# Performance work log

Measured on AMD Instinct MI355X. Metric: run time of the kernel, lower is better.

The kernel has to match this reference:

```python
import math
import jax, jax.numpy as jnp
import numpy as np

D_MODEL = 1024
N_HEADS = 16
D_K = D_MODEL // N_HEADS
THETA = 10000.0
B, S = 2, 2048


def setup_inputs() -> dict:
    key = jax.random.key(0)
    k1, k2, k3 = jax.random.split(key, 3)
    x = jax.random.normal(k1, (B, S, D_MODEL), dtype=jnp.float32)
    token_positions = jnp.arange(B * S, dtype=jnp.int32).reshape(B, S)
    std_qkv = math.sqrt(2.0 / (D_MODEL + 3 * D_MODEL))
    std_o = math.sqrt(2.0 / (D_MODEL + D_MODEL))
    W_qkv = jax.random.truncated_normal(k2, -3.0, 3.0, (3 * D_MODEL, D_MODEL), dtype=jnp.float32) * std_qkv
    W_o = jax.random.truncated_normal(k3, -3.0, 3.0, (D_MODEL, D_MODEL), dtype=jnp.float32) * std_o
    return {"x": x, "W_qkv": W_qkv, "W_o": W_o, "token_positions": token_positions}


def _rope(x, pos):
    # x: (B, H, S, D_K); pos: (B, S) int
    half = D_K // 2
    inv_freq = 1.0 / (THETA ** (jnp.arange(0, D_K, 2, dtype=jnp.float32) / D_K))  # (half,)
    # pos_extended = pos[:, None, :] -> freqs (B, 1, S, half)
    freqs = pos[:, None, :, None].astype(jnp.float32) * inv_freq
    cos, sin = jnp.cos(freqs), jnp.sin(freqs)
    xr = x.reshape(*x.shape[:-1], half, 2)
    x1, x2 = xr[..., 0], xr[..., 1]
    out = jnp.stack([x1 * cos - x2 * sin, x2 * cos + x1 * sin], axis=-1)
    return out.reshape(x.shape)


def reference(x, W_qkv, W_o, token_positions):
    seq_len = x.shape[-2]
    qkv = jnp.einsum('bsi,oi->bso', x, W_qkv)
    q, k, v = jnp.split(qkv, 3, axis=-1)
    # (B, S, H*D) -> (B, H, S, D)
    def to_heads(t):
        return t.reshape(t.shape[0], t.shape[1], N_HEADS, D_K).transpose(0, 2, 1, 3)
    q, k, v = to_heads(q), to_heads(k), to_heads(v)
    q = _rope(q, token_positions)
    k = _rope(k, token_positions)
    scores = jnp.einsum('bhnd,bhmd->bhnm', q, k) / math.sqrt(D_K)
    causal = jnp.tril(jnp.ones((seq_len, seq_len), dtype=bool))
    scores = jnp.where(causal, scores, -jnp.inf)
    attn = jax.nn.softmax(scores, axis=-1)
    out = jnp.einsum('bhnm,bhmd->bhnd', attn, v)
    out = out.transpose(0, 2, 1, 3).reshape(x.shape[0], seq_len, D_MODEL)
    return jnp.einsum('bsi,oi->bso', out, W_o)
```

## Files before the change

kernel.cpp:

```cpp
#include <hip/hip_runtime.h>
#include <cmath>

typedef __bf16 bf16;
typedef bf16 bf16x4 __attribute__((ext_vector_type(4)));
typedef bf16 bf16x8 __attribute__((ext_vector_type(8)));
typedef float f32x4 __attribute__((ext_vector_type(4)));

#define MFMA16(a, b, c) __builtin_amdgcn_mfma_f32_16x16x32_bf16(a, b, c, 0, 0, 0)

#define GLOAD16(g, l)                                                   \
  __builtin_amdgcn_global_load_lds(                                     \
      (const __attribute__((address_space(1))) unsigned int*)(g),       \
      (__attribute__((address_space(3))) unsigned int*)(l), 16, 0, 0)

__global__ __launch_bounds__(256) void cvt_all(
    const float* __restrict__ x, const float* __restrict__ wqkv,
    const float* __restrict__ wo, bf16* __restrict__ xb,
    bf16* __restrict__ wqkvb, bf16* __restrict__ wob) {
  int i = (blockIdx.x * 256 + threadIdx.x) * 4;
  const float* src;
  bf16* dst;
  if (i < (4 << 20)) {
    src = x + i; dst = xb + i;
  } else if (i < (7 << 20)) {
    src = wqkv + (i - (4 << 20)); dst = wqkvb + (i - (4 << 20));
  } else {
    src = wo + (i - (7 << 20)); dst = wob + (i - (7 << 20));
  }
  const f32x4 v = *(const f32x4*)src;
  bf16x4 o = {(bf16)v[0], (bf16)v[1], (bf16)v[2], (bf16)v[3]};
  *(bf16x4*)dst = o;
}

template <int EPI, int BN>
__global__ __launch_bounds__(256) void gemm_nt(
    const bf16* __restrict__ A, const bf16* __restrict__ Bm,
    const int* __restrict__ tokpos,
    bf16* __restrict__ out0, bf16* __restrict__ out1, bf16* __restrict__ out2,
    float* __restrict__ outF, int N) {
  constexpr int NI = BN / 32;
  constexpr int TSTRIDE = 136;
  __shared__ __align__(16) union SMem {
    struct { bf16 A[2][128 * 32]; bf16 B[2][BN * 32]; } st;
    bf16 T[EPI ? 128 * TSTRIDE : 1];
  } sm;
  const int tid = threadIdx.x;
  const int w = tid >> 6, lane = tid & 63, quad = lane >> 4, m16 = lane & 15;
  const int nwg = gridDim.x * gridDim.y;
  int bid = blockIdx.y * gridDim.x + blockIdx.x;
  bid = (bid & 7) * (nwg >> 3) + (bid >> 3);
  const int m0 = (bid / gridDim.x) * 128, n0 = (bid % gridDim.x) * BN;
  const int wm = (w >> 1) * 64, wn = (w & 1) * (BN / 2);

  f32x4 acc[4][NI] = {};

  const int row0 = tid >> 2, ch = tid & 3;
  const bf16* Ag0 = A + (size_t)(m0 + row0) * 1024 + ch * 8;
  const bf16* Ag1 = Ag0 + (size_t)64 * 1024;
  const bf16* Bg0 = Bm + (size_t)(n0 + row0) * 1024 + ch * 8;
  const bf16* Bg1 = Bg0 + (size_t)64 * 1024;

  auto STAGE = [&](int p, int k0) {
    GLOAD16(Ag0 + k0, &sm.st.A[p][tid * 8]);
    GLOAD16(Ag1 + k0, &sm.st.A[p][2048 + tid * 8]);
    GLOAD16(Bg0 + k0, &sm.st.B[p][tid * 8]);
    if constexpr (BN == 128) GLOAD16(Bg1 + k0, &sm.st.B[p][2048 + tid * 8]);
  };

  STAGE(0, 0);
  __syncthreads();

  int p = 0;
  for (int k0 = 0; k0 < 1024; k0 += 32) {
    const bool more = (k0 + 32) < 1024;
    if (more) STAGE(p ^ 1, k0 + 32);
    bf16x8 af[4], bfr[NI];
#pragma unroll
    for (int mi = 0; mi < 4; ++mi)
      af[mi] =
          *(const bf16x8*)(&sm.st.A[p][(wm + mi * 16 + m16) * 32 + quad * 8]);
#pragma unroll
    for (int ni = 0; ni < NI; ++ni)
      bfr[ni] =
          *(const bf16x8*)(&sm.st.B[p][(wn + ni * 16 + m16) * 32 + quad * 8]);
#pragma unroll
    for (int mi = 0; mi < 4; ++mi)
#pragma unroll
      for (int ni = 0; ni < NI; ++ni)
        acc[mi][ni] = MFMA16(af[mi], bfr[ni], acc[mi][ni]);
    if (more) {
      __syncthreads();
      p ^= 1;
    }
  }

  if constexpr (EPI == 0) {
#pragma unroll
    for (int mi = 0; mi < 4; ++mi) {
      int rowb = m0 + wm + mi * 16 + quad * 4;
#pragma unroll
      for (int r = 0; r < 4; ++r) {
        size_t off = (size_t)(rowb + r) * N + n0 + wn;
#pragma unroll
        for (int ni = 0; ni < NI; ++ni)
          outF[off + ni * 16 + m16] = acc[mi][ni][r];
      }
    }
  } else {
    const int secb = n0 >> 10;
    if (secb == 2) {
      __syncthreads();
#pragma unroll
      for (int mi = 0; mi < 4; ++mi) {
        int rlb = wm + mi * 16 + quad * 4;
#pragma unroll
        for (int ni = 0; ni < 4; ++ni) {
          int c = wn + ni * 16 + m16;
          bf16x4 pk = {(bf16)acc[mi][ni][0], (bf16)acc[mi][ni][1],
                       (bf16)acc[mi][ni][2], (bf16)acc[mi][ni][3]};
          *(bf16x4*)(&sm.T[c * TSTRIDE + rlb]) = pk;
        }
      }
      __syncthreads();
      const int bb = m0 >> 11, S0 = m0 & 2047;
      const size_t base = ((size_t)bb * 1024 + (n0 - 2048)) * 2048 + S0;
#pragma unroll
      for (int it = 0; it < 8; ++it) {
        int chunk = it * 256 + tid;
        int c = chunk >> 4, kp = (chunk & 15) * 8;
        bf16x8 v = *(const bf16x8*)(&sm.T[c * TSTRIDE + kp]);
        *(bf16x8*)(out2 + base + (size_t)c * 2048 + kp) = v;
      }
    } else {
      bf16* dst = secb ? out1 : out0;
      const float sc = secb ? 1.0f : 0.125f;
#pragma unroll
      for (int mi = 0; mi < 4; ++mi) {
        int rowb = m0 + wm + mi * 16 + quad * 4;
        int pos4[4];
#pragma unroll
        for (int r = 0; r < 4; ++r) pos4[r] = tokpos[rowb + r];
#pragma unroll
        for (int ni = 0; ni < 4; ++ni) {
          int col = n0 + wn + ni * 16 + m16;
          int f = col & 1023, h = f >> 6, d = f & 63;
          float inv = __expf(-(float)(d & ~1) * (9.2103403719762f / 64.f));
#pragma unroll
          for (int r = 0; r < 4; ++r) {
            float v = acc[mi][ni][r];
            float vp = __shfl_xor(v, 1);
            float ang = (float)pos4[r] * inv;
            float cs, sn;
            __sincosf(ang, &sn, &cs);
            float ov = (d & 1) ? (v * cs + vp * sn) : (v * cs - vp * sn);
            ov *= sc;
            int row = rowb + r;
            int bb = row >> 11, s = row & 2047;
            dst[((size_t)(bb * 16 + h) * 2048 + s) * 64 + d] = (bf16)ov;
          }
        }
      }
    }
  }
}

__global__ __launch_bounds__(256) void attn_kernel(
    const bf16* __restrict__ Q, const bf16* __restrict__ K,
    const bf16* __restrict__ Vt, bf16* __restrict__ O) {
  __shared__ __align__(16) bf16 KP[2][64 * 64];
  __shared__ __align__(16) bf16 VP[2][64 * 64];
  __shared__ __align__(16) bf16 PS[4][16 * 64];
  const int tid = threadIdx.x;
  const int w = tid >> 6, lane = tid & 63, quad = lane >> 4, m16 = lane & 15;
  const int h8 = m16 >> 3, ml = m16 & 7;
  const int bh = blockIdx.x;
  const int j = 31 - blockIdx.y;
  const bf16* Qb = Q + (size_t)bh * 2048 * 64;
  const bf16* Kb = K + (size_t)bh * 2048 * 64;
  const bf16* Vb = Vt + (size_t)bh * 64 * 2048;

  const int srow = tid >> 3, sc = (tid & 7) ^ (srow & 7);
  const bf16* Kg = Kb + (size_t)srow * 64 + sc * 8;
  const bf16* Vg = Vb + (size_t)srow * 2048 + sc * 8;
  auto GSTAGE = [&](int kt, int p) {
    const bf16* kg = Kg + (size_t)kt * 4096;
    const bf16* vg = Vg + kt * 64;
    GLOAD16(kg, &KP[p][tid * 8]);
    GLOAD16(kg + (size_t)32 * 64, &KP[p][2048 + tid * 8]);
    GLOAD16(vg, &VP[p][tid * 8]);
    GLOAD16(vg + (size_t)32 * 2048, &VP[p][2048 + tid * 8]);
  };

  const bf16* qrow = Qb + (size_t)(j * 64 + w * 16 + m16) * 64;
  bf16x8 aq[2];
  aq[0] = *(const bf16x8*)(qrow + quad * 8);
  aq[1] = *(const bf16x8*)(qrow + 32 + quad * 8);

  GSTAGE(0, 0);
  __syncthreads();

  f32x4 o[4] = {};
  float l4[4] = {0.f, 0.f, 0.f, 0.f};
  const int qrel = w * 16 + quad * 4;
  bf16* ps = PS[w];

  int p = 0;
  for (int kt = 0; kt <= j; ++kt) {
    const bool more = kt < j;
    if (more) GSTAGE(kt + 1, p ^ 1);

    f32x4 sa[4] = {};
    __builtin_amdgcn_s_setprio(1);
#pragma unroll
    for (int kk = 0; kk < 2; ++kk)
#pragma unroll
      for (int ni = 0; ni < 4; ++ni) {
        bf16x8 bk = *(const bf16x8*)(
            &KP[p][(ni * 16 + m16) * 64 + (((kk * 4 + quad) ^ ml) << 3)]);
        sa[ni] = MFMA16(aq[kk], bk, sa[ni]);
      }
    __builtin_amdgcn_s_setprio(0);

    const bool diag = (kt == j);
#pragma unroll
    for (int r = 0; r < 4; ++r) {
      const int prow = quad * 4 + r;
      const int rb = prow * 64, rx = prow & 7;
#pragma unroll
      for (int ni = 0; ni < 4; ++ni) {
        float pp = exp2f(fmaf(sa[ni][r], 1.44269504f, -11.5415603f));
        if (diag && (ni * 16 + m16) > qrel + r) pp = 0.f;
        l4[r] += pp;
        ps[rb + (((ni * 2 + h8) ^ rx) << 3) + ml] = (bf16)pp;
      }
    }
    bf16x8 ap[2];
#pragma unroll
    for (int kk = 0; kk < 2; ++kk)
      ap[kk] =
          *(const bf16x8*)(&ps[m16 * 64 + (((kk * 4 + quad) ^ ml) << 3)]);
    __builtin_amdgcn_s_setprio(1);
#pragma unroll
    for (int kk = 0; kk < 2; ++kk)
#pragma unroll
      for (int ng = 0; ng < 4; ++ng) {
        bf16x8 bv = *(const bf16x8*)(
            &VP[p][(ng * 16 + m16) * 64 + (((kk * 4 + quad) ^ ml) << 3)]);
        o[ng] = MFMA16(ap[kk], bv, o[ng]);
      }
    __builtin_amdgcn_s_setprio(0);

    if (more) {
      __syncthreads();
      p ^= 1;
    }
  }

  const int b = bh >> 4, hh = bh & 15;
#pragma unroll
  for (int r = 0; r < 4; ++r) {
    float l = l4[r];
    l += __shfl_xor(l, 1);
    l += __shfl_xor(l, 2);
    l += __shfl_xor(l, 4);
    l += __shfl_xor(l, 8);
    float inv_l = 1.f / l;
    int s = j * 64 + w * 16 + quad * 4 + r;
    size_t rowoff = (size_t)(b * 2048 + s) * 1024 + hh * 64;
#pragma unroll
    for (int ng = 0; ng < 4; ++ng)
      O[rowoff + ng * 16 + m16] = (bf16)(o[ng][r] * inv_l);
  }
}

extern "C" void kernel_launch(void* const* d_in, const int* in_sizes, int n_in,
                              void* d_out, int out_size, void* d_ws, size_t ws_size,
                              hipStream_t stream) {
  (void)in_sizes; (void)n_in; (void)out_size; (void)ws_size;
  const float* x = (const float*)d_in[0];
  const float* Wqkv = (const float*)d_in[1];
  const float* Wo = (const float*)d_in[2];
  const int* tokpos = (const int*)d_in[3];
  float* out = (float*)d_out;

  const size_t NEL = (size_t)2 * 16 * 2048 * 64;
  bf16* Qws = (bf16*)d_ws;
  bf16* Kws = Qws + NEL;
  bf16* Vtw = Kws + NEL;
  bf16* Ows = Vtw + NEL;
  bf16* xb  = Ows + NEL;
  bf16* Wqkvb = xb + NEL;
  bf16* Wob = Wqkvb + (size_t)3072 * 1024;

  cvt_all<<<8192, 256, 0, stream>>>(x, Wqkv, Wo, xb, Wqkvb, Wob);

  gemm_nt<1, 128><<<dim3(24, 32), 256, 0, stream>>>(xb, Wqkvb, tokpos, Qws,
                                                    Kws, Vtw, nullptr, 3072);
  attn_kernel<<<dim3(32, 32), 256, 0, stream>>>(Qws, Kws, Vtw, Ows);
  gemm_nt<0, 64><<<dim3(16, 32), 256, 0, stream>>>(Ows, Wob, nullptr, nullptr,
                                                   nullptr, nullptr, out, 1024);
}
```

Baseline: 176.9 us.

## Precompute RoPE cos/sin table and stage Q/K epilogue through LDS for vector stores

The conversion kernel gains extra blocks that precompute a cos/sin table indexed by position and frequency, written into the attention-output workspace before that buffer is used. The QKV GEMM epilogue reads this table instead of calling exp and sincos per element. It then writes rotated Q/K values into shared memory and emits coalesced 16-byte stores per head row, replacing scattered 2-byte stores. The trade-off is extra table reads and two barriers. The table assumes positions below 4096, since it is sized for 4096 positions × 32 frequencies.

```diff
diff --git a/kernel.cpp b/kernel.cpp
--- a/kernel.cpp
+++ b/kernel.cpp
@@ -16,7 +16,17 @@
 __global__ __launch_bounds__(256) void cvt_all(
     const float* __restrict__ x, const float* __restrict__ wqkv,
     const float* __restrict__ wo, bf16* __restrict__ xb,
-    bf16* __restrict__ wqkvb, bf16* __restrict__ wob) {
+    bf16* __restrict__ wqkvb, bf16* __restrict__ wob,
+    float2* __restrict__ tab) {
+  if (blockIdx.x >= 8192) {
+    int id = (blockIdx.x - 8192) * 256 + threadIdx.x;
+    int pos = id >> 5, dh = id & 31;
+    float ang = (float)pos * __expf(-(float)dh * 0.28782313662425572f);
+    float sn, cs;
+    __sincosf(ang, &sn, &cs);
+    tab[id] = make_float2(cs, sn);
+    return;
+  }
   int i = (blockIdx.x * 256 + threadIdx.x) * 4;
   const float* src;
   bf16* dst;
@@ -35,7 +45,7 @@
 template <int EPI, int BN>
 __global__ __launch_bounds__(256) void gemm_nt(
     const bf16* __restrict__ A, const bf16* __restrict__ Bm,
-    const int* __restrict__ tokpos,
+    const int* __restrict__ tokpos, const float2* __restrict__ tab,
     bf16* __restrict__ out0, bf16* __restrict__ out1, bf16* __restrict__ out2,
     float* __restrict__ outF, int N) {
   constexpr int NI = BN / 32;
@@ -108,6 +118,7 @@
     }
   } else {
     const int secb = n0 >> 10;
+    const int bb = m0 >> 11, S0 = m0 & 2047;
     if (secb == 2) {
       __syncthreads();
 #pragma unroll
@@ -122,7 +133,6 @@
         }
       }
       __syncthreads();
-      const int bb = m0 >> 11, S0 = m0 & 2047;
       const size_t base = ((size_t)bb * 1024 + (n0 - 2048)) * 2048 + S0;
 #pragma unroll
       for (int it = 0; it < 8; ++it) {
@@ -132,33 +142,40 @@
         *(bf16x8*)(out2 + base + (size_t)c * 2048 + kp) = v;
       }
     } else {
+      __syncthreads();
       bf16* dst = secb ? out1 : out0;
       const float sc = secb ? 1.0f : 0.125f;
 #pragma unroll
       for (int mi = 0; mi < 4; ++mi) {
-        int rowb = m0 + wm + mi * 16 + quad * 4;
+        int rlb = wm + mi * 16 + quad * 4;
         int pos4[4];
 #pragma unroll
-        for (int r = 0; r < 4; ++r) pos4[r] = tokpos[rowb + r];
+        for (int r = 0; r < 4; ++r) pos4[r] = tokpos[m0 + rlb + r];
 #pragma unroll
         for (int ni = 0; ni < 4; ++ni) {
-          int col = n0 + wn + ni * 16 + m16;
-          int f = col & 1023, h = f >> 6, d = f & 63;
-          float inv = __expf(-(float)(d & ~1) * (9.2103403719762f / 64.f));
+          int c = wn + ni * 16 + m16;
+          int dh = (c & 63) >> 1;
 #pragma unroll
           for (int r = 0; r < 4; ++r) {
             float v = acc[mi][ni][r];
             float vp = __shfl_xor(v, 1);
-            float ang = (float)pos4[r] * inv;
-            float cs, sn;
-            __sincosf(ang, &sn, &cs);
-            float ov = (d & 1) ? (v * cs + vp * sn) : (v * cs - vp * sn);
-            ov *= sc;
-            int row = rowb + r;
-            int bb = row >> 11, s = row & 2047;
-            dst[((size_t)(bb * 16 + h) * 2048 + s) * 64 + d] = (bf16)ov;
+            float2 cssn = tab[pos4[r] * 32 + dh];
+            float ov = (c & 1) ? (v * cssn.x + vp * cssn.y)
+                               : (v * cssn.x - vp * cssn.y);
+            sm.T[(rlb + r) * TSTRIDE + c] = (bf16)(ov * sc);
           }
         }
+      }
+      __syncthreads();
+      const int hbase = (n0 & 1023) >> 6;
+#pragma unroll
+      for (int it = 0; it < 8; ++it) {
+        int chunk = it * 256 + tid;
+        int sl = chunk >> 4, part = chunk & 15;
+        int h = hbase + (part >> 3), d0 = (part & 7) * 8;
+        bf16x8 v = *(const bf16x8*)(&sm.T[sl * TSTRIDE + part * 8]);
+        *(bf16x8*)(dst + ((size_t)(bb * 16 + h) * 2048 + S0 + sl) * 64 + d0) =
+            v;
       }
     }
   }
@@ -291,12 +308,15 @@
   bf16* xb  = Ows + NEL;
   bf16* Wqkvb = xb + NEL;
   bf16* Wob = Wqkvb + (size_t)3072 * 1024;
-
-  cvt_all<<<8192, 256, 0, stream>>>(x, Wqkv, Wo, xb, Wqkvb, Wob);
-
-  gemm_nt<1, 128><<<dim3(24, 32), 256, 0, stream>>>(xb, Wqkvb, tokpos, Qws,
-                                                    Kws, Vtw, nullptr, 3072);
+  float2* tab = (float2*)Ows;
+
+  cvt_all<<<8704, 256, 0, stream>>>(x, Wqkv, Wo, xb, Wqkvb, Wob, tab);
+
+  gemm_nt<1, 128><<<dim3(24, 32), 256, 0, stream>>>(xb, Wqkvb, tokpos, tab,
+                                                    Qws, Kws, Vtw, nullptr,
+                                                    3072);
   attn_kernel<<<dim3(32, 32), 256, 0, stream>>>(Qws, Kws, Vtw, Ows);
   gemm_nt<0, 64><<<dim3(16, 32), 256, 0, stream>>>(Ows, Wob, nullptr, nullptr,
-                                                   nullptr, nullptr, out, 1024);
+                                                   nullptr, nullptr, nullptr,
+                                                   out, 1024);
 }
```

Measured after the change: 187.3 us. +5.9%, slower.

## Pair causal query tiles per block to balance work and share K/V loads

Applied to the files above, without the earlier changes.

Each attention block now handles two query tiles, jA and 31-jA, so every block does the same causal work and each staged K/V tile feeds both tiles while the short one is still active. The grid is halved to 32x16 and the P scratch buffer doubles to hold both tiles. This removes the load imbalance of the triangular causal mask and reduces K/V global and LDS traffic per query. In exchange it uses more registers and LDS and leaves half as many blocks, which may lower occupancy and latency hiding.

```diff
diff --git a/kernel.cpp b/kernel.cpp
--- a/kernel.cpp
+++ b/kernel.cpp
@@ -169,12 +169,12 @@
     const bf16* __restrict__ Vt, bf16* __restrict__ O) {
   __shared__ __align__(16) bf16 KP[2][64 * 64];
   __shared__ __align__(16) bf16 VP[2][64 * 64];
-  __shared__ __align__(16) bf16 PS[4][16 * 64];
+  __shared__ __align__(16) bf16 PS[8][16 * 64];
   const int tid = threadIdx.x;
   const int w = tid >> 6, lane = tid & 63, quad = lane >> 4, m16 = lane & 15;
   const int h8 = m16 >> 3, ml = m16 & 7;
   const int bh = blockIdx.x;
-  const int j = 31 - blockIdx.y;
+  const int jA = blockIdx.y, jB = 31 - jA;
   const bf16* Qb = Q + (size_t)bh * 2048 * 64;
   const bf16* Kb = K + (size_t)bh * 2048 * 64;
   const bf16* Vb = Vt + (size_t)bh * 64 * 2048;
@@ -191,37 +191,24 @@
     GLOAD16(vg + (size_t)32 * 2048, &VP[p][2048 + tid * 8]);
   };
 
-  const bf16* qrow = Qb + (size_t)(j * 64 + w * 16 + m16) * 64;
-  bf16x8 aq[2];
-  aq[0] = *(const bf16x8*)(qrow + quad * 8);
-  aq[1] = *(const bf16x8*)(qrow + 32 + quad * 8);
+  const bf16* qrowA = Qb + (size_t)(jA * 64 + w * 16 + m16) * 64;
+  const bf16* qrowB = Qb + (size_t)(jB * 64 + w * 16 + m16) * 64;
+  bf16x8 aqA[2], aqB[2];
+  aqA[0] = *(const bf16x8*)(qrowA + quad * 8);
+  aqA[1] = *(const bf16x8*)(qrowA + 32 + quad * 8);
+  aqB[0] = *(const bf16x8*)(qrowB + quad * 8);
+  aqB[1] = *(const bf16x8*)(qrowB + 32 + quad * 8);
 
   GSTAGE(0, 0);
   __syncthreads();
 
-  f32x4 o[4] = {};
-  float l4[4] = {0.f, 0.f, 0.f, 0.f};
+  f32x4 oA[4] = {}, oB[4] = {};
+  float lA[4] = {0.f, 0.f, 0.f, 0.f}, lB[4] = {0.f, 0.f, 0.f, 0.f};
   const int qrel = w * 16 + quad * 4;
-  bf16* ps = PS[w];
-
-  int p = 0;
-  for (int kt = 0; kt <= j; ++kt) {
-    const bool more = kt < j;
-    if (more) GSTAGE(kt + 1, p ^ 1);
-
-    f32x4 sa[4] = {};
-    __builtin_amdgcn_s_setprio(1);
-#pragma unroll
-    for (int kk = 0; kk < 2; ++kk)
-#pragma unroll
-      for (int ni = 0; ni < 4; ++ni) {
-        bf16x8 bk = *(const bf16x8*)(
-            &KP[p][(ni * 16 + m16) * 64 + (((kk * 4 + quad) ^ ml) << 3)]);
-        sa[ni] = MFMA16(aq[kk], bk, sa[ni]);
-      }
-    __builtin_amdgcn_s_setprio(0);
-
-    const bool diag = (kt == j);
+  bf16* psA = PS[w];
+  bf16* psB = PS[4 + w];
+
+  auto SOFTMAX = [&](const f32x4* sa, float* lp, bf16* ps, bool diag) {
 #pragma unroll
     for (int r = 0; r < 4; ++r) {
       const int prow = quad * 4 + r;
@@ -230,24 +217,76 @@
       for (int ni = 0; ni < 4; ++ni) {
         float pp = exp2f(fmaf(sa[ni][r], 1.44269504f, -11.5415603f));
         if (diag && (ni * 16 + m16) > qrel + r) pp = 0.f;
-        l4[r] += pp;
+        lp[r] += pp;
         ps[rb + (((ni * 2 + h8) ^ rx) << 3) + ml] = (bf16)pp;
       }
     }
-    bf16x8 ap[2];
+  };
+  auto READAP = [&](const bf16* ps, bf16x8* ap) {
 #pragma unroll
     for (int kk = 0; kk < 2; ++kk)
       ap[kk] =
           *(const bf16x8*)(&ps[m16 * 64 + (((kk * 4 + quad) ^ ml) << 3)]);
+  };
+
+  int p = 0;
+  for (int kt = 0; kt <= jB; ++kt) {
+    const bool more = kt < jB;
+    const bool actA = kt <= jA;
+    if (more) GSTAGE(kt + 1, p ^ 1);
+
+    f32x4 saA[4] = {}, saB[4] = {};
     __builtin_amdgcn_s_setprio(1);
-#pragma unroll
-    for (int kk = 0; kk < 2; ++kk)
-#pragma unroll
-      for (int ng = 0; ng < 4; ++ng) {
-        bf16x8 bv = *(const bf16x8*)(
-            &VP[p][(ng * 16 + m16) * 64 + (((kk * 4 + quad) ^ ml) << 3)]);
-        o[ng] = MFMA16(ap[kk], bv, o[ng]);
-      }
+    if (actA) {
+#pragma unroll
+      for (int kk = 0; kk < 2; ++kk)
+#pragma unroll
+        for (int ni = 0; ni < 4; ++ni) {
+          bf16x8 bk = *(const bf16x8*)(
+              &KP[p][(ni * 16 + m16) * 64 + (((kk * 4 + quad) ^ ml) << 3)]);
+          saB[ni] = MFMA16(aqB[kk], bk, saB[ni]);
+          saA[ni] = MFMA16(aqA[kk], bk, saA[ni]);
+        }
+    } else {
+#pragma unroll
+      for (int kk = 0; kk < 2; ++kk)
+#pragma unroll
+        for (int ni = 0; ni < 4; ++ni) {
+          bf16x8 bk = *(const bf16x8*)(
+              &KP[p][(ni * 16 + m16) * 64 + (((kk * 4 + quad) ^ ml) << 3)]);
+          saB[ni] = MFMA16(aqB[kk], bk, saB[ni]);
+        }
+    }
+    __builtin_amdgcn_s_setprio(0);
+
+    SOFTMAX(saB, lB, psB, kt == jB);
+    if (actA) SOFTMAX(saA, lA, psA, kt == jA);
+
+    bf16x8 apA[2], apB[2];
+    READAP(psB, apB);
+    if (actA) READAP(psA, apA);
+
+    __builtin_amdgcn_s_setprio(1);
+    if (actA) {
+#pragma unroll
+      for (int kk = 0; kk < 2; ++kk)
+#pragma unroll
+        for (int ng = 0; ng < 4; ++ng) {
+          bf16x8 bv = *(const bf16x8*)(
+              &VP[p][(ng * 16 + m16) * 64 + (((kk * 4 + quad) ^ ml) << 3)]);
+          oB[ng] = MFMA16(apB[kk], bv, oB[ng]);
+          oA[ng] = MFMA16(apA[kk], bv, oA[ng]);
+        }
+    } else {
+#pragma unroll
+      for (int kk = 0; kk < 2; ++kk)
+#pragma unroll
+        for (int ng = 0; ng < 4; ++ng) {
+          bf16x8 bv = *(const bf16x8*)(
+              &VP[p][(ng * 16 + m16) * 64 + (((kk * 4 + quad) ^ ml) << 3)]);
+          oB[ng] = MFMA16(apB[kk], bv, oB[ng]);
+        }
+    }
     __builtin_amdgcn_s_setprio(0);
 
     if (more) {
@@ -257,20 +296,24 @@
   }
 
   const int b = bh >> 4, hh = bh & 15;
-#pragma unroll
-  for (int r = 0; r < 4; ++r) {
-    float l = l4[r];
-    l += __shfl_xor(l, 1);
-    l += __shfl_xor(l, 2);
-    l += __shfl_xor(l, 4);
-    l += __shfl_xor(l, 8);
-    float inv_l = 1.f / l;
-    int s = j * 64 + w * 16 + quad * 4 + r;
-    size_t rowoff = (size_t)(b * 2048 + s) * 1024 + hh * 64;
-#pragma unroll
-    for (int ng = 0; ng < 4; ++ng)
-      O[rowoff + ng * 16 + m16] = (bf16)(o[ng][r] * inv_l);
-  }
+  auto EPI = [&](const f32x4* o, const float* lp, int q0) {
+#pragma unroll
+    for (int r = 0; r < 4; ++r) {
+      float l = lp[r];
+      l += __shfl_xor(l, 1);
+      l += __shfl_xor(l, 2);
+      l += __shfl_xor(l, 4);
+      l += __shfl_xor(l, 8);
+      float inv_l = 1.f / l;
+      int s = q0 + w * 16 + quad * 4 + r;
+      size_t rowoff = (size_t)(b * 2048 + s) * 1024 + hh * 64;
+#pragma unroll
+      for (int ng = 0; ng < 4; ++ng)
+        O[rowoff + ng * 16 + m16] = (bf16)(o[ng][r] * inv_l);
+    }
+  };
+  EPI(oA, lA, jA * 64);
+  EPI(oB, lB, jB * 64);
 }
 
 extern "C" void kernel_launch(void* const* d_in, const int* in_sizes, int n_in,
@@ -296,7 +339,7 @@
 
   gemm_nt<1, 128><<<dim3(24, 32), 256, 0, stream>>>(xb, Wqkvb, tokpos, Qws,
                                                     Kws, Vtw, nullptr, 3072);
-  attn_kernel<<<dim3(32, 32), 256, 0, stream>>>(Qws, Kws, Vtw, Ows);
+  attn_kernel<<<dim3(32, 16), 256, 0, stream>>>(Qws, Kws, Vtw, Ows);
   gemm_nt<0, 64><<<dim3(16, 32), 256, 0, stream>>>(Ows, Wob, nullptr, nullptr,
                                                    nullptr, nullptr, out, 1024);
 }
```

New measurement: 189.1 us. 1.07x slower.
